# Kernel optimization log

Measured on AMD Instinct MI355X. Metric: run time of the kernel, lower is better.

Reference implementation:

```python
import jax, jax.numpy as jnp
import numpy as np

EPS = 0.05
N = 33554432  # 2**25 annotation steps


def setup_inputs() -> dict:
    key = jax.random.key(0)
    # categories in 1..5 (cat==0 is a no-op skip in the original loop; excluding it
    # keeps the output length static at N+1)
    annotation_series = jax.random.randint(key, (N,), 1, 6, dtype=jnp.int64 if jax.config.jax_enable_x64 else jnp.int32)
    # learned scalar weights of the six Linear(1,1,bias=False) layers, at their init constants
    return {
        "annotation_series": annotation_series,
        "origin_w": jnp.asarray(0.0, jnp.float32),
        "big_decrease_w": jnp.asarray(-0.3, jnp.float32),
        "decrease_w": jnp.asarray(-0.1, jnp.float32),
        "same_w": jnp.asarray(0.0, jnp.float32),
        "increase_w": jnp.asarray(0.1, jnp.float32),
        "big_increase_w": jnp.asarray(0.3, jnp.float32),
    }


def _change_table(origin_w, bd, d, s, inc, bi):
    sg = jax.lax.stop_gradient  # clamp bounds came from .item() in torch -> detached
    c1 = jnp.minimum(bd, sg(jnp.minimum(0.0, d))) - EPS                 # big decrease
    c2 = jnp.clip(d, sg(bd) + EPS, 0.0 - EPS)                           # decrease
    c3 = s                                                              # same
    c4 = jnp.clip(inc, 0.0 + EPS, sg(bi) - EPS)                         # increase
    c5 = jnp.maximum(bi, sg(jnp.maximum(0.0, inc)) + EPS)               # big increase
    zero = jnp.zeros_like(c1)  # cat 0 unused (inputs restricted to 1..5)
    return jnp.stack([zero, c1, c2, c3, c4, c5])  # [6]


def reference(annotation_series, origin_w, big_decrease_w, decrease_w, same_w, increase_w, big_increase_w):
    table = _change_table(origin_w, big_decrease_w, decrease_w, same_w, increase_w, big_increase_w)
    changes = table[annotation_series]                    # [N] gather from 6-entry LUT
    series = origin_w + jnp.cumsum(changes)               # [N] inclusive prefix sum
    return jnp.concatenate([origin_w[None], series])      # [N+1]
```

## Files before the change

### kernel.cpp

```cpp
#include <hip/hip_runtime.h>

#define EPS_C 0.05f
#define BLOCK 256
#define CHUNK 4096

__device__ __forceinline__ void build_table(const float* bd_p, const float* d_p,
                                            const float* s_p, const float* inc_p,
                                            const float* bi_p, float* cs) {
  if (threadIdx.x == 0) {
    float bd = *bd_p, d = *d_p, s = *s_p, inc = *inc_p, bi = *bi_p;
    cs[0] = 0.0f;
    cs[1] = fminf(bd, fminf(0.0f, d)) - EPS_C;
    cs[2] = fminf(fmaxf(d, bd + EPS_C), -EPS_C);
    cs[3] = s;
    cs[4] = fminf(fmaxf(inc, EPS_C), bi - EPS_C);
    cs[5] = fmaxf(bi, fmaxf(0.0f, inc) + EPS_C);
    cs[6] = 0.0f; cs[7] = 0.0f;
  }
}

__global__ __launch_bounds__(BLOCK) void k_reduce_pack(
    const int* __restrict__ ann, const float* bd, const float* d,
    const float* s, const float* inc, const float* bi,
    uint2* __restrict__ packed, float* __restrict__ sums) {
  __shared__ float cs[8];
  __shared__ float wsum[BLOCK / 64];
  build_table(bd, d, s, inc, bi, cs);
  __syncthreads();

  const int b = blockIdx.x, t = threadIdx.x;
  const int4* in4 = (const int4*)(ann + (size_t)b * CHUNK);

  unsigned int w0 = 0u, w1 = 0u;
  float sum = 0.0f;
#pragma unroll
  for (int i = 0; i < 4; ++i) {
    int4 v = in4[t * 4 + i];
    sum += cs[v.x] + cs[v.y] + cs[v.z] + cs[v.w];
    unsigned int nib = (unsigned)v.x | ((unsigned)v.y << 4) |
                       ((unsigned)v.z << 8) | ((unsigned)v.w << 12);
    if (i < 2) w0 |= nib << ((i & 1) * 16);
    else       w1 |= nib << ((i & 1) * 16);
  }
  packed[(size_t)b * BLOCK + t] = make_uint2(w0, w1);

#pragma unroll
  for (int off = 32; off >= 1; off >>= 1) sum += __shfl_down(sum, off, 64);
  const int lane = t & 63, wid = t >> 6;
  if (lane == 0) wsum[wid] = sum;
  __syncthreads();
  if (t == 0) sums[b] = wsum[0] + wsum[1] + wsum[2] + wsum[3];
}

__global__ __launch_bounds__(BLOCK) void k_scan_out(
    const uint2* __restrict__ packed, const float* __restrict__ sums,
    const float* __restrict__ origin, const float* bd, const float* d,
    const float* s, const float* inc, const float* bi,
    float* __restrict__ out, int nb) {
  __shared__ float cs[8];
  __shared__ float wsum[BLOCK / 64];
  __shared__ float s_base;
  build_table(bd, d, s, inc, bi, cs);
  __syncthreads();

  const int b = blockIdx.x, t = threadIdx.x;
  const int lane = t & 63, wid = t >> 6;

  float p = 0.0f;
  for (int i = t; i < b; i += BLOCK) p += sums[i];
#pragma unroll
  for (int off = 32; off >= 1; off >>= 1) p += __shfl_down(p, off, 64);
  if (lane == 0) wsum[wid] = p;
  __syncthreads();
  if (t == 0) s_base = *origin + wsum[0] + wsum[1] + wsum[2] + wsum[3];
  __syncthreads();

  uint2 w = packed[(size_t)b * BLOCK + t];
  float vals[16];
#pragma unroll
  for (int j = 0; j < 8; ++j) vals[j] = cs[(w.x >> (4 * j)) & 0xF];
#pragma unroll
  for (int j = 0; j < 8; ++j) vals[8 + j] = cs[(w.y >> (4 * j)) & 0xF];

  float run = 0.0f;
#pragma unroll
  for (int i = 0; i < 16; ++i) run += vals[i];

  float x = run;
#pragma unroll
  for (int off = 1; off < 64; off <<= 1) {
    float y = __shfl_up(x, off, 64);
    if (lane >= off) x += y;
  }
  __syncthreads();
  if (lane == 63) wsum[wid] = x;
  __syncthreads();
  float wexcl = 0.0f;
#pragma unroll
  for (int i = 0; i < BLOCK / 64; ++i)
    if (i < wid) wexcl += wsum[i];

  const float off0 = s_base + wexcl + (x - run);

  const size_t base = (size_t)b * CHUNK;
  float4* out4 = (float4*)(out + base);
  float r = off0;
#pragma unroll
  for (int i = 0; i < 4; ++i) {
    float4 o;
    o.x = r; r += vals[i * 4 + 0];
    o.y = r; r += vals[i * 4 + 1];
    o.z = r; r += vals[i * 4 + 2];
    o.w = r; r += vals[i * 4 + 3];
    out4[t * 4 + i] = o;
  }
  if (b == nb - 1 && t == BLOCK - 1)
    out[(size_t)nb * CHUNK] = r;
}

extern "C" void kernel_launch(void* const* d_in, const int* in_sizes, int n_in,
                              void* d_out, int out_size, void* d_ws, size_t ws_size,
                              hipStream_t stream) {
  const int*   ann    = (const int*)d_in[0];
  const float* origin = (const float*)d_in[1];
  const float* bd     = (const float*)d_in[2];
  const float* dw     = (const float*)d_in[3];
  const float* sw     = (const float*)d_in[4];
  const float* inc    = (const float*)d_in[5];
  const float* bi     = (const float*)d_in[6];
  float* out = (float*)d_out;

  const int N  = in_sizes[0];
  const int nb = N / CHUNK;

  float* sums   = (float*)d_ws;
  uint2* packed = (uint2*)((char*)d_ws + 32768);

  k_reduce_pack<<<nb, BLOCK, 0, stream>>>(ann, bd, dw, sw, inc, bi, packed, sums);
  k_scan_out<<<nb, BLOCK, 0, stream>>>(packed, sums, origin, bd, dw, sw, inc, bi,
                                       out, nb);
}
```

Baseline: 274.1 us.

## Double per-block chunk, carry scan across sub-tiles, use nontemporal output stores

Each block now handles two 4096-element sub-tiles, so the block count halves. That shrinks the quadratic serial prefix-over-block-sums loop in the scan kernel and cuts per-block overhead. The scan kernel prefetches its packed words before the base-offset reduction, carries the running total between sub-tiles, and writes output with nontemporal stores to avoid polluting the cache. The cost is an extra pair of barriers per sub-tile and fewer blocks available for latency hiding.

```diff
diff --git a/kernel.cpp b/kernel.cpp
--- a/kernel.cpp
+++ b/kernel.cpp
@@ -2,7 +2,10 @@
 
 #define EPS_C 0.05f
 #define BLOCK 256
-#define CHUNK 4096
+#define SUBT 2
+#define CHUNK (SUBT * 4096)
+
+typedef float f4 __attribute__((ext_vector_type(4)));
 
 __device__ __forceinline__ void build_table(const float* bd_p, const float* d_p,
                                             const float* s_p, const float* inc_p,
@@ -31,18 +34,21 @@
   const int b = blockIdx.x, t = threadIdx.x;
   const int4* in4 = (const int4*)(ann + (size_t)b * CHUNK);
 
-  unsigned int w0 = 0u, w1 = 0u;
   float sum = 0.0f;
 #pragma unroll
-  for (int i = 0; i < 4; ++i) {
-    int4 v = in4[t * 4 + i];
-    sum += cs[v.x] + cs[v.y] + cs[v.z] + cs[v.w];
-    unsigned int nib = (unsigned)v.x | ((unsigned)v.y << 4) |
-                       ((unsigned)v.z << 8) | ((unsigned)v.w << 12);
-    if (i < 2) w0 |= nib << ((i & 1) * 16);
-    else       w1 |= nib << ((i & 1) * 16);
+  for (int j = 0; j < SUBT; ++j) {
+    unsigned int w0 = 0u, w1 = 0u;
+#pragma unroll
+    for (int i = 0; i < 4; ++i) {
+      int4 v = in4[j * 1024 + t * 4 + i];
+      sum += cs[v.x] + cs[v.y] + cs[v.z] + cs[v.w];
+      unsigned int nib = (unsigned)v.x | ((unsigned)v.y << 4) |
+                         ((unsigned)v.z << 8) | ((unsigned)v.w << 12);
+      if (i < 2) w0 |= nib << ((i & 1) * 16);
+      else       w1 |= nib << ((i & 1) * 16);
+    }
+    packed[(size_t)b * (SUBT * BLOCK) + j * BLOCK + t] = make_uint2(w0, w1);
   }
-  packed[(size_t)b * BLOCK + t] = make_uint2(w0, w1);
 
 #pragma unroll
   for (int off = 32; off >= 1; off >>= 1) sum += __shfl_down(sum, off, 64);
@@ -66,6 +72,11 @@
   const int b = blockIdx.x, t = threadIdx.x;
   const int lane = t & 63, wid = t >> 6;
 
+  uint2 w[SUBT];
+#pragma unroll
+  for (int j = 0; j < SUBT; ++j)
+    w[j] = packed[(size_t)b * (SUBT * BLOCK) + j * BLOCK + t];
+
   float p = 0.0f;
   for (int i = t; i < b; i += BLOCK) p += sums[i];
 #pragma unroll
@@ -75,47 +86,53 @@
   if (t == 0) s_base = *origin + wsum[0] + wsum[1] + wsum[2] + wsum[3];
   __syncthreads();
 
-  uint2 w = packed[(size_t)b * BLOCK + t];
-  float vals[16];
+  float carry = s_base;
 #pragma unroll
-  for (int j = 0; j < 8; ++j) vals[j] = cs[(w.x >> (4 * j)) & 0xF];
+  for (int j = 0; j < SUBT; ++j) {
+    float vals[16];
 #pragma unroll
-  for (int j = 0; j < 8; ++j) vals[8 + j] = cs[(w.y >> (4 * j)) & 0xF];
+    for (int k = 0; k < 8; ++k) vals[k] = cs[(w[j].x >> (4 * k)) & 0xF];
+#pragma unroll
+    for (int k = 0; k < 8; ++k) vals[8 + k] = cs[(w[j].y >> (4 * k)) & 0xF];
 
-  float run = 0.0f;
+    float run = 0.0f;
 #pragma unroll
-  for (int i = 0; i < 16; ++i) run += vals[i];
+    for (int i = 0; i < 16; ++i) run += vals[i];
 
-  float x = run;
+    float x = run;
 #pragma unroll
-  for (int off = 1; off < 64; off <<= 1) {
-    float y = __shfl_up(x, off, 64);
-    if (lane >= off) x += y;
+    for (int off = 1; off < 64; off <<= 1) {
+      float y = __shfl_up(x, off, 64);
+      if (lane >= off) x += y;
+    }
+    __syncthreads();
+    if (lane == 63) wsum[wid] = x;
+    __syncthreads();
+    float wexcl = 0.0f, tot = 0.0f;
+#pragma unroll
+    for (int i = 0; i < BLOCK / 64; ++i) {
+      float wv = wsum[i];
+      if (i < wid) wexcl += wv;
+      tot += wv;
+    }
+    const float off0 = carry + wexcl + (x - run);
+
+    f4* out4 = (f4*)(out + (size_t)b * CHUNK + j * 4096);
+    float r = off0;
+#pragma unroll
+    for (int i = 0; i < 4; ++i) {
+      f4 o;
+      o.x = r; r += vals[i * 4 + 0];
+      o.y = r; r += vals[i * 4 + 1];
+      o.z = r; r += vals[i * 4 + 2];
+      o.w = r; r += vals[i * 4 + 3];
+      __builtin_nontemporal_store(o, &out4[t * 4 + i]);
+    }
+    carry += tot;
+
+    if (b == nb - 1 && t == BLOCK - 1 && j == SUBT - 1)
+      out[(size_t)nb * CHUNK] = r;
   }
-  __syncthreads();
-  if (lane == 63) wsum[wid] = x;
-  __syncthreads();
-  float wexcl = 0.0f;
-#pragma unroll
-  for (int i = 0; i < BLOCK / 64; ++i)
-    if (i < wid) wexcl += wsum[i];
-
-  const float off0 = s_base + wexcl + (x - run);
-
-  const size_t base = (size_t)b * CHUNK;
-  float4* out4 = (float4*)(out + base);
-  float r = off0;
-#pragma unroll
-  for (int i = 0; i < 4; ++i) {
-    float4 o;
-    o.x = r; r += vals[i * 4 + 0];
-    o.y = r; r += vals[i * 4 + 1];
-    o.z = r; r += vals[i * 4 + 2];
-    o.w = r; r += vals[i * 4 + 3];
-    out4[t * 4 + i] = o;
-  }
-  if (b == nb - 1 && t == BLOCK - 1)
-    out[(size_t)nb * CHUNK] = r;
 }
 
 extern "C" void kernel_launch(void* const* d_in, const int* in_sizes, int n_in,
```

New measurement: 410.4 us. 1.5x slower.
